# Kernel tuning notes

Hardware: AMD Instinct MI355X
Metric: run time of the kernel (lower is better)

The kernel has to match this reference:

```python
import jax, jax.numpy as jnp
import numpy as np

OBS, SEQ = 8, 12          # observed steps, predicted steps (seq_len init arg)
G, P = 96, 16             # scenes x pedestrians per scene (uniform groups)
B = G * P                 # 1536
H, E, BOT, MID = 128, 64, 1024, 512


def setup_inputs() -> dict:
    key = jax.random.key(0)
    ks = jax.random.split(key, 26)
    rn = lambda k, sh, s=0.05: jax.random.normal(k, sh, jnp.float32) * s
    starts = jnp.arange(G, dtype=jnp.int64) * P
    return {
        "obs_traj": rn(ks[0], (OBS, B, 2), 1.0),
        "obs_traj_rel": rn(ks[1], (OBS, B, 2), 1.0),
        "typeID_seq": rn(ks[2], (OBS, B, 1), 1.0),
        "h0": rn(ks[3], (1, B, H), 0.1),
        "c0": rn(ks[4], (1, B, H), 0.1),
        "seq_start_end": jnp.stack([starts, starts + P], axis=1),
        # decoder spatial embedding Linear(2, E)
        "W_emb": rn(ks[5], (E, 2)), "b_emb": rn(ks[6], (E,)),
        # LSTM(E, H) weights, gate order i,f,g,o (PyTorch convention)
        "W_ih": rn(ks[7], (4 * H, E)), "b_ih": rn(ks[8], (4 * H,)),
        "W_hh": rn(ks[9], (4 * H, H)), "b_hh": rn(ks[10], (4 * H,)),
        # hidden2pos Linear(H, 2)
        "W_pos": rn(ks[11], (2, H)), "b_pos": rn(ks[12], (2,)),
        # PoolHiddenNet: spatial_embedding Linear(2, E), mlp_pre_pool [E+H, 512, BOT]
        "Wp_emb": rn(ks[13], (E, 2)), "bp_emb": rn(ks[14], (E,)),
        "Wp1": rn(ks[15], (MID, E + H)), "bp1": rn(ks[16], (MID,)),
        "Wp2": rn(ks[17], (BOT, MID)), "bp2": rn(ks[18], (BOT,)),
        # Decoder mlp [H+BOT, mlp_dim, H]
        "Wm1": rn(ks[19], (1024, H + BOT)), "bm1": rn(ks[20], (1024,)),
        "Wm2": rn(ks[21], (H, 1024)), "bm2": rn(ks[22], (H,)),
    }


def _forward(obs_traj, obs_traj_rel, h0, c0,
             W_emb, b_emb, W_ih, b_ih, W_hh, b_hh, W_pos, b_pos,
             Wp_emb, bp_emb, Wp1, bp1, Wp2, bp2, Wm1, bm1, Wm2, bm2):
    batch = obs_traj.shape[1]

    def pool(h, pos):
        # uniform groups: h_states.view(-1,H)[start:end] == reshape to (G,P,H)
        hh = h.reshape(G, P, H)
        pp = pos.reshape(G, P, 2)
        # torch semantics: row (i,j) holds pos[j]-pos[i] and hidden[j]
        rel = pp[:, None, :, :] - pp[:, :, None, :]          # (G,Pi,Pj,2)
        emb = rel @ Wp_emb.T + bp_emb                        # (G,Pi,Pj,E)
        hb = jnp.broadcast_to(hh[:, None, :, :], (G, P, P, H))
        x = jnp.concatenate([emb, hb], axis=-1)              # (G,Pi,Pj,E+H)
        x = jax.nn.relu(x @ Wp1.T + bp1)
        x = jax.nn.relu(x @ Wp2.T + bp2)                     # (G,Pi,Pj,BOT)
        return x.max(axis=2).reshape(batch, BOT)             # max over neighbors j

    def step(carry, _):
        h, c, last_pos, dec_in = carry
        gates = dec_in @ W_ih.T + b_ih + h @ W_hh.T + b_hh
        i, f, g, o = jnp.split(gates, 4, axis=-1)
        c = jax.nn.sigmoid(f) * c + jax.nn.sigmoid(i) * jnp.tanh(g)
        h = jax.nn.sigmoid(o) * jnp.tanh(c)
        rel_pos = h @ W_pos.T + b_pos                        # (B,2)
        curr_pos = rel_pos + last_pos
        pool_h = pool(h, curr_pos)
        ctx = jnp.concatenate([h, pool_h], axis=-1)          # (B,H+BOT)
        h = jax.nn.relu(jax.nn.relu(ctx @ Wm1.T + bm1) @ Wm2.T + bm2)
        dec_in = rel_pos @ W_emb.T + b_emb
        return (h, c, curr_pos, dec_in), rel_pos

    dec_in0 = obs_traj_rel[-1] @ W_emb.T + b_emb
    carry0 = (h0[0], c0[0], obs_traj[-1], dec_in0)
    (h, c, _, _), rels = jax.lax.scan(step, carry0, None, length=SEQ)
    return rels, h[None]                                     # (SEQ,B,2), (1,B,H)


def reference(obs_traj, obs_traj_rel, typeID_seq, h0, c0, seq_start_end,
              W_emb, b_emb, W_ih, b_ih, W_hh, b_hh, W_pos, b_pos,
              Wp_emb, bp_emb, Wp1, bp1, Wp2, bp2, Wm1, bm1, Wm2, bm2):
    # typeID_seq / seq_start_end unused math-wise (typeID module off; groups uniform)
    return _forward(obs_traj, obs_traj_rel, h0, c0,
                    W_emb, b_emb, W_ih, b_ih, W_hh, b_hh, W_pos, b_pos,
                    Wp_emb, bp_emb, Wp1, bp1, Wp2, bp2, Wm1, bm1, Wm2, bm2)
```

## Files before the change

### kernel.cpp

```cpp
#include <hip/hip_runtime.h>
#include <hip/hip_bf16.h>
#include <math.h>

#define OBS 8
#define SEQL 12
#define G 96
#define PP 16
#define B 1536
#define HD 128
#define ED 64
#define BOT 1024
#define MIDD 512
#define CTXD (HD + BOT)
#define MLPH 1024

typedef __attribute__((ext_vector_type(8))) short bf16x8;
typedef __attribute__((ext_vector_type(4))) float f32x4;

__device__ inline short f2bf(float x) {
    union { float f; unsigned u; } v; v.f = x;
    unsigned r = v.u + 0x7fffu + ((v.u >> 16) & 1u);
    return (short)(r >> 16);
}

__device__ inline unsigned pk2bf(float a, float b) {
    union { __hip_bfloat162 h; unsigned u; } c;
    c.h = __float22bfloat162_rn(float2{a, b});
    return c.u;
}

__global__ void swizzleB_kernel(const float* __restrict__ src, unsigned short* __restrict__ dst,
                                int NT, int K, int total) {
    int u = blockIdx.x * 256 + threadIdx.x;
    if (u >= total) return;
    int l = u & 63; int v = u >> 6; int nt = v % NT; int kt = v / NT;
    int n = nt * 16 + (l & 15);
    int k = kt * 32 + ((l >> 4) << 3);
    const float* s = src + n * K + k;
    float4 s0 = *(const float4*)s;
    float4 s1 = *(const float4*)(s + 4);
    bf16x8 o;
    o[0] = f2bf(s0.x); o[1] = f2bf(s0.y); o[2] = f2bf(s0.z); o[3] = f2bf(s0.w);
    o[4] = f2bf(s1.x); o[5] = f2bf(s1.y); o[6] = f2bf(s1.z); o[7] = f2bf(s1.w);
    *(bf16x8*)(dst + u * 8) = o;
}

__global__ void swizzle_cat_kernel(const float* __restrict__ W_ih, const float* __restrict__ W_hh,
                                   unsigned short* __restrict__ dst) {
    int u = blockIdx.x * 256 + threadIdx.x;
    if (u >= 6 * 32 * 64) return;
    int l = u & 63; int v = u >> 6; int nt = v & 31; int kt = v >> 5;
    int n = nt * 16 + (l & 15);
    int k0 = kt * 32 + ((l >> 4) << 3);
    bf16x8 o;
#pragma unroll
    for (int e = 0; e < 8; ++e) {
        int k = k0 + e;
        float val = (k < ED) ? W_ih[n * ED + k] : W_hh[n * HD + (k - ED)];
        o[e] = f2bf(val);
    }
    *(bf16x8*)(dst + u * 8) = o;
}

__global__ void swizzle_p1_kernel(const float* __restrict__ Wp1,
                                  const float* __restrict__ CV,
                                  unsigned short* __restrict__ dst) {
    int u = blockIdx.x * 256 + threadIdx.x;
    if (u >= 5 * 32 * 64) return;
    int l = u & 63; int v = u >> 6; int nt = v & 31; int kt = v >> 5;
    int n = nt * 16 + (l & 15);
    int k0 = kt * 32 + ((l >> 4) << 3);
    bf16x8 o;
#pragma unroll
    for (int e = 0; e < 8; ++e) {
        int k = k0 + e;
        float val;
        if (k < HD)           val = Wp1[n * (ED + HD) + ED + k];
        else if (k == HD + 2) val = CV[n];
        else                  val = 0.f;
        o[e] = f2bf(val);
    }
    *(bf16x8*)(dst + u * 8) = o;
}

__global__ void mcvec_kernel(const float* __restrict__ Wp1, const float* __restrict__ Wp_emb,
                             const float* __restrict__ bp_emb, const float* __restrict__ bp1,
                             float* __restrict__ M0, float* __restrict__ M1, float* __restrict__ CV) {
    int r = blockIdx.x * blockDim.x + threadIdx.x;
    if (r >= MIDD) return;
    float m0 = 0.f, m1 = 0.f, cv = 0.f;
    for (int e = 0; e < ED; ++e) {
        float w = Wp1[r * (ED + HD) + e];
        m0 += w * Wp_emb[e * 2 + 0];
        m1 += w * Wp_emb[e * 2 + 1];
        cv += w * bp_emb[e];
    }
    M0[r] = m0; M1[r] = m1; CV[r] = cv + bp1[r];
}

__global__ void m01f_kernel(const float* __restrict__ M0, const float* __restrict__ M1,
                            float* __restrict__ M0F, float* __restrict__ M1F) {
    int id = blockIdx.x * 256 + threadIdx.x;
    if (id >= 16 * 64 * 8) return;
    int e = id & 7;
    int lane = (id >> 3) & 63;
    int kt = id >> 9;
    int k = kt * 32 + ((lane >> 4) << 3) + e;
    M0F[id] = M0[k];
    M1F[id] = M1[k];
}

__global__ void init_kernel(const float* __restrict__ obs_traj, const float* __restrict__ obs_traj_rel,
                            const float* __restrict__ h0, const float* __restrict__ c0,
                            const float* __restrict__ W_emb, const float* __restrict__ b_emb,
                            float* __restrict__ Hb, float* __restrict__ Cb,
                            float* __restrict__ POSb, float* __restrict__ DIN) {
    int b = blockIdx.x;
    int t = threadIdx.x;
    Hb[b * HD + t] = h0[b * HD + t];
    Cb[b * HD + t] = c0[b * HD + t];
    if (t < 2) POSb[b * 2 + t] = obs_traj[((OBS - 1) * B + b) * 2 + t];
    if (t < ED) {
        float rx = obs_traj_rel[((OBS - 1) * B + b) * 2 + 0];
        float ry = obs_traj_rel[((OBS - 1) * B + b) * 2 + 1];
        DIN[b * ED + t] = W_emb[t * 2 + 0] * rx + W_emb[t * 2 + 1] * ry + b_emb[t];
    }
}

__global__ __launch_bounds__(512) void step_kernel(
    const unsigned short* __restrict__ WcatF, const float* __restrict__ b_ih,
    const float* __restrict__ b_hh,
    const float* __restrict__ W_pos, const float* __restrict__ b_pos,
    const float* __restrict__ W_emb, const float* __restrict__ b_emb,
    const unsigned short* __restrict__ Wp1F2,
    float* __restrict__ Hb, float* __restrict__ Cb, float* __restrict__ POSb,
    float* __restrict__ DIN, unsigned short* __restrict__ Hbf,
    float* __restrict__ AbF, float* __restrict__ rel_out) {

    __shared__ unsigned short gf[6 * 64 * 8];
    __shared__ unsigned short a2f[5 * 64 * 8];
    __shared__ float hsh[16 * HD];
    __shared__ float relsh[16][4];

    int gsc = blockIdx.x;
    int t = threadIdx.x;
    int lane = t & 63, w = t >> 6;
    int colid = lane & 15, quad = lane >> 4;

    if (t < 384) {
        int kt = t >> 6;
        int j = lane & 15;
        int b = gsc * PP + j;
        int k0 = kt * 32 + ((lane >> 4) << 3);
        float4 x0, x1;
        if (k0 < ED) {
            const float4* p = (const float4*)(DIN + b * ED + k0);
            x0 = p[0]; x1 = p[1];
        } else {
            const float4* p = (const float4*)(Hb + b * HD + (k0 - ED));
            x0 = p[0]; x1 = p[1];
        }
        union { bf16x8 v; unsigned u32[4]; } o;
        o.u32[0] = pk2bf(x0.x, x0.y);
        o.u32[1] = pk2bf(x0.z, x0.w);
        o.u32[2] = pk2bf(x1.x, x1.y);
        o.u32[3] = pk2bf(x1.z, x1.w);
        *(bf16x8*)(gf + t * 8) = o.v;
    }
    __syncthreads();

    f32x4 acc[4];
#pragma unroll
    for (int gi = 0; gi < 4; ++gi) acc[gi] = (f32x4)0.f;
#pragma unroll
    for (int kt = 0; kt < 6; ++kt) {
        bf16x8 af = *(const bf16x8*)(gf + (kt * 64 + lane) * 8);
#pragma unroll
        for (int gi = 0; gi < 4; ++gi) {
            bf16x8 bfr = *(const bf16x8*)(WcatF + ((kt * 32 + gi * 8 + w) * 64 + lane) * 8);
            acc[gi] = __builtin_amdgcn_mfma_f32_16x16x32_bf16(af, bfr, acc[gi], 0, 0, 0);
        }
    }
    int hcol = w * 16 + colid;
    float bias[4];
#pragma unroll
    for (int gi = 0; gi < 4; ++gi) {
        int n = (gi * 8 + w) * 16 + colid;
        bias[gi] = b_ih[n] + b_hh[n];
    }
#pragma unroll
    for (int r = 0; r < 4; ++r) {
        int row = quad * 4 + r;
        int b = gsc * PP + row;
        float gI = acc[0][r] + bias[0];
        float gF = acc[1][r] + bias[1];
        float gG = acc[2][r] + bias[2];
        float gO = acc[3][r] + bias[3];
        float c = Cb[b * HD + hcol];
        float cn = (1.f / (1.f + expf(-gF))) * c + (1.f / (1.f + expf(-gI))) * tanhf(gG);
        float hn = (1.f / (1.f + expf(-gO))) * tanhf(cn);
        Cb[b * HD + hcol] = cn;
        Hbf[b * HD + hcol] = (unsigned short)f2bf(hn);
        hsh[row * HD + hcol] = hn;
    }
    __syncthreads();

    {
        int row = t >> 5, kk = t & 31;
        float r0 = 0.f, r1 = 0.f;
#pragma unroll
        for (int q = 0; q < 4; ++q) {
            int k = kk + q * 32;
            float hv = hsh[row * HD + k];
            r0 = fmaf(hv, W_pos[k], r0);
            r1 = fmaf(hv, W_pos[HD + k], r1);
        }
#pragma unroll
        for (int m = 16; m >= 1; m >>= 1) {
            r0 += __shfl_xor(r0, m, 64);
            r1 += __shfl_xor(r1, m, 64);
        }
        if (kk == 0) {
            int b = gsc * PP + row;
            r0 += b_pos[0]; r1 += b_pos[1];
            float px = POSb[b * 2 + 0] + r0;
            float py = POSb[b * 2 + 1] + r1;
            POSb[b * 2 + 0] = px; POSb[b * 2 + 1] = py;
            rel_out[b * 2 + 0] = r0; rel_out[b * 2 + 1] = r1;
            relsh[row][0] = r0; relsh[row][1] = r1; relsh[row][2] = px; relsh[row][3] = py;
        }
    }
    __syncthreads();

#pragma unroll
    for (int rep = 0; rep < 2; ++rep) {
        int idx = rep * 512 + t;
        int row = idx >> 6, e = idx & 63;
        int b = gsc * PP + row;
        DIN[b * ED + e] = W_emb[e * 2 + 0] * relsh[row][0] +
                          W_emb[e * 2 + 1] * relsh[row][1] + b_emb[e];
    }
    if (t < 320) {
        int kt = t >> 6;
        int j = lane & 15;
        int k0 = kt * 32 + ((lane >> 4) << 3);
        float e8[8];
#pragma unroll
        for (int e = 0; e < 8; ++e) {
            int k = k0 + e;
            float v;
            if (k < HD)            v = hsh[j * HD + k];
            else if (k == HD + 2)  v = 1.f;
            else                   v = 0.f;
            e8[e] = v;
        }
        union { bf16x8 v; unsigned u32[4]; } o;
        o.u32[0] = pk2bf(e8[0], e8[1]);
        o.u32[1] = pk2bf(e8[2], e8[3]);
        o.u32[2] = pk2bf(e8[4], e8[5]);
        o.u32[3] = pk2bf(e8[6], e8[7]);
        *(bf16x8*)(a2f + t * 8) = o.v;
    }
    __syncthreads();

    f32x4 acc2[4];
#pragma unroll
    for (int q = 0; q < 4; ++q) acc2[q] = (f32x4)0.f;
#pragma unroll
    for (int kt = 0; kt < 5; ++kt) {
        bf16x8 af = *(const bf16x8*)(a2f + (kt * 64 + lane) * 8);
#pragma unroll
        for (int q = 0; q < 4; ++q) {
            bf16x8 bfr = *(const bf16x8*)(Wp1F2 + ((kt * 32 + w * 4 + q) * 64 + lane) * 8);
            acc2[q] = __builtin_amdgcn_mfma_f32_16x16x32_bf16(af, bfr, acc2[q], 0, 0, 0);
        }
    }
#pragma unroll
    for (int q = 0; q < 4; ++q)
#pragma unroll
        for (int r = 0; r < 4; ++r) {
            int j = quad * 4 + r;
            int k = (w * 4 + q) * 16 + colid;
            int kt2 = k >> 5, lk = (k >> 3) & 3, e = k & 7;
            AbF[((gsc * 16 + kt2) * 64 + lk * 16 + j) * 8 + e] = acc2[q][r];
        }
}

__global__ __launch_bounds__(256, 4) void pool_gemm13_kernel(
    const float* __restrict__ AbF, const float* __restrict__ POSb,
    const float* __restrict__ M0F, const float* __restrict__ M1F,
    const unsigned short* __restrict__ Wp2F, const float* __restrict__ bp2,
    unsigned short* __restrict__ POOLbf) {

    __shared__ __align__(16) unsigned short Bst[2][8 * 64 * 8];
    __shared__ __align__(16) float UMst[2][6][64 * 4];

    int bi = blockIdx.x;
    int g = bi % 96;
    int rest = bi / 96;
    int io = rest >> 3;
    int colq = rest & 7;
    int t = threadIdx.x, lane = t & 63, w = t >> 6;
    int i0 = io * 8 + w * 2;
    int j = lane & 15;
    int ntb = colq * 8;

    float pjx = POSb[(g * PP + j) * 2 + 0];
    float pjy = POSb[(g * PP + j) * 2 + 1];
    float dx[2], dy[2];
#pragma unroll
    for (int p = 0; p < 2; ++p) {
        int gi = g * PP + i0 + p;
        dx[p] = pjx - POSb[gi * 2 + 0];
        dy[p] = pjy - POSb[gi * 2 + 1];
    }

    const float* ag = AbF + (size_t)g * (16 * 64 * 8);

    auto stage = [&](int kt, int buf) {
#pragma unroll
        for (int r = 0; r < 2; ++r) {
            int u = r * 256 + t;
            int nt = u >> 6, l = u & 63;
            *(bf16x8*)&Bst[buf][u * 8] =
                *(const bf16x8*)(Wp2F + ((kt * 64 + ntb + nt) * 64 + l) * 8);
        }
        {
            int pt = t >> 6;
            int l = t & 63;
            const float* src = (pt < 2) ? (ag + kt * 512 + l * 8 + pt * 4)
                                        : (M0F + kt * 512 + l * 8 + (pt - 2) * 4);
            *(float4*)&UMst[buf][pt][l * 4] = *(const float4*)src;
            if (t < 128) {
                int pt2 = 4 + (t >> 6);
                *(float4*)&UMst[buf][pt2][l * 4] =
                    *(const float4*)(M1F + kt * 512 + l * 8 + (t >> 6) * 4);
            }
        }
    };

    f32x4 acc[2][8];
#pragma unroll
    for (int p = 0; p < 2; ++p)
#pragma unroll
        for (int n = 0; n < 8; ++n) acc[p][n] = (f32x4)0.f;

    stage(0, 0);
    __syncthreads();

    for (int kt = 0; kt < 16; ++kt) {
        int buf = kt & 1;
        if (kt < 15) stage(kt + 1, buf ^ 1);

        float4 u0  = *(const float4*)&UMst[buf][0][lane * 4];
        float4 u1  = *(const float4*)&UMst[buf][1][lane * 4];
        float4 m00 = *(const float4*)&UMst[buf][2][lane * 4];
        float4 m01 = *(const float4*)&UMst[buf][3][lane * 4];
        float4 m10 = *(const float4*)&UMst[buf][4][lane * 4];
        float4 m11 = *(const float4*)&UMst[buf][5][lane * 4];

        bf16x8 af[2];
#pragma unroll
        for (int p = 0; p < 2; ++p) {
            float dxp = dx[p], dyp = dy[p];
            float r0 = fmaxf(fmaf(m10.x, dyp, fmaf(m00.x, dxp, u0.x)), 0.f);
            float r1 = fmaxf(fmaf(m10.y, dyp, fmaf(m00.y, dxp, u0.y)), 0.f);
            float r2 = fmaxf(fmaf(m10.z, dyp, fmaf(m00.z, dxp, u0.z)), 0.f);
            float r3 = fmaxf(fmaf(m10.w, dyp, fmaf(m00.w, dxp, u0.w)), 0.f);
            float r4 = fmaxf(fmaf(m11.x, dyp, fmaf(m01.x, dxp, u1.x)), 0.f);
            float r5 = fmaxf(fmaf(m11.y, dyp, fmaf(m01.y, dxp, u1.y)), 0.f);
            float r6 = fmaxf(fmaf(m11.z, dyp, fmaf(m01.z, dxp, u1.z)), 0.f);
            float r7 = fmaxf(fmaf(m11.w, dyp, fmaf(m01.w, dxp, u1.w)), 0.f);
            union { bf16x8 v; unsigned u32[4]; } o;
            o.u32[0] = pk2bf(r0, r1);
            o.u32[1] = pk2bf(r2, r3);
            o.u32[2] = pk2bf(r4, r5);
            o.u32[3] = pk2bf(r6, r7);
            af[p] = o.v;
        }
#pragma unroll
        for (int ng = 0; ng < 2; ++ng) {
            bf16x8 bfr[4];
#pragma unroll
            for (int n = 0; n < 4; ++n)
                bfr[n] = *(const bf16x8*)&Bst[buf][((ng * 4 + n) * 64 + lane) * 8];
#pragma unroll
            for (int n = 0; n < 4; ++n) {
                acc[0][ng * 4 + n] =
                    __builtin_amdgcn_mfma_f32_16x16x32_bf16(af[0], bfr[n], acc[0][ng * 4 + n], 0, 0, 0);
                acc[1][ng * 4 + n] =
                    __builtin_amdgcn_mfma_f32_16x16x32_bf16(af[1], bfr[n], acc[1][ng * 4 + n], 0, 0, 0);
            }
        }
        __syncthreads();
    }

    int quad = lane >> 4, colid = lane & 15;
#pragma unroll
    for (int p = 0; p < 2; ++p) {
        int i = g * PP + i0 + p;
#pragma unroll
        for (int n = 0; n < 8; ++n) {
            float m = fmaxf(fmaxf(acc[p][n][0], acc[p][n][1]),
                            fmaxf(acc[p][n][2], acc[p][n][3]));
            m = fmaxf(m, __shfl_xor(m, 16, 64));
            m = fmaxf(m, __shfl_xor(m, 32, 64));
            if (quad == 0) {
                int col = (ntb + n) * 16 + colid;
                float v = fmaxf(m + bp2[col], 0.f);
                POOLbf[i * BOT + col] = (unsigned short)f2bf(v);
            }
        }
    }
}

__global__ __launch_bounds__(256) void mlp1_mfma_kernel(
    const unsigned short* __restrict__ Hbf, const unsigned short* __restrict__ POOLbf,
    const unsigned short* __restrict__ Wm1F, const float* __restrict__ bm1,
    unsigned short* __restrict__ Y1Mbf) {

    __shared__ unsigned short a_f[16 * 64 * 8];
    int mg = blockIdx.x;
    int ng = blockIdx.y;
    int t = threadIdx.x, lane = t & 63, w = t >> 6;
    int rh = w >> 1, nh = w & 1;

    f32x4 acc[2][2];
#pragma unroll
    for (int a = 0; a < 2; ++a)
#pragma unroll
        for (int b = 0; b < 2; ++b) acc[a][b] = (f32x4)0.f;

    for (int c = 0; c < 9; ++c) {
        __syncthreads();
#pragma unroll
        for (int u0 = 0; u0 < 1024; u0 += 256) {
            int u = u0 + t;
            int rg = u >> 8, kt = (u >> 6) & 3, l = u & 63;
            int row = mg * 64 + rg * 16 + (l & 15);
            int kl = kt * 32 + ((l >> 4) << 3);
            const unsigned short* src = (c == 0) ? (Hbf + row * HD + kl)
                                                 : (POOLbf + row * BOT + (c - 1) * 128 + kl);
            *(bf16x8*)(a_f + u * 8) = *(const bf16x8*)src;
        }
        __syncthreads();
#pragma unroll
        for (int kt = 0; kt < 4; ++kt) {
            int ktg = c * 4 + kt;
            bf16x8 bfr[2];
#pragma unroll
            for (int j = 0; j < 2; ++j) {
                int ntg = ng * 4 + nh * 2 + j;
                bfr[j] = *(const bf16x8*)(Wm1F + ((ktg * 64 + ntg) * 64 + lane) * 8);
            }
#pragma unroll
            for (int ri = 0; ri < 2; ++ri) {
                int rg = rh * 2 + ri;
                bf16x8 af = *(const bf16x8*)(a_f + ((rg * 4 + kt) * 64 + lane) * 8);
#pragma unroll
                for (int j = 0; j < 2; ++j)
                    acc[ri][j] = __builtin_amdgcn_mfma_f32_16x16x32_bf16(af, bfr[j], acc[ri][j], 0, 0, 0);
            }
        }
    }
    int quad = lane >> 4, colid = lane & 15;
#pragma unroll
    for (int ri = 0; ri < 2; ++ri)
#pragma unroll
        for (int j = 0; j < 2; ++j) {
            int col = ng * 64 + (nh * 2 + j) * 16 + colid;
            float bb = bm1[col];
#pragma unroll
            for (int r = 0; r < 4; ++r) {
                int row = mg * 64 + (rh * 2 + ri) * 16 + quad * 4 + r;
                float v = fmaxf(acc[ri][j][r] + bb, 0.f);
                Y1Mbf[row * MLPH + col] = (unsigned short)f2bf(v);
            }
        }
}

__global__ __launch_bounds__(256) void mlp2_mfma_kernel(
    const unsigned short* __restrict__ Y1Mbf, const unsigned short* __restrict__ Wm2F,
    const float* __restrict__ bm2, float* __restrict__ Hb, float* __restrict__ hout) {

    __shared__ unsigned short a_f[32 * 64 * 8];
    int rg = blockIdx.x;
    int t = threadIdx.x, lane = t & 63, w = t >> 6;

#pragma unroll
    for (int u0 = 0; u0 < 2048; u0 += 256) {
        int u = u0 + t;
        int kt = u >> 6, l = u & 63;
        int row = rg * 16 + (l & 15);
        int kl = kt * 32 + ((l >> 4) << 3);
        *(bf16x8*)(a_f + u * 8) = *(const bf16x8*)(Y1Mbf + row * MLPH + kl);
    }
    __syncthreads();

    f32x4 acc[2];
    acc[0] = (f32x4)0.f; acc[1] = (f32x4)0.f;
    for (int kt = 0; kt < 32; ++kt) {
        bf16x8 af = *(const bf16x8*)(a_f + (kt * 64 + lane) * 8);
#pragma unroll
        for (int j = 0; j < 2; ++j) {
            int ntg = w * 2 + j;
            bf16x8 bfr = *(const bf16x8*)(Wm2F + ((kt * 8 + ntg) * 64 + lane) * 8);
            acc[j] = __builtin_amdgcn_mfma_f32_16x16x32_bf16(af, bfr, acc[j], 0, 0, 0);
        }
    }
    int quad = lane >> 4, colid = lane & 15;
#pragma unroll
    for (int j = 0; j < 2; ++j) {
        int col = (w * 2 + j) * 16 + colid;
        float bb = bm2[col];
#pragma unroll
        for (int r = 0; r < 4; ++r) {
            int row = rg * 16 + quad * 4 + r;
            float v = fmaxf(acc[j][r] + bb, 0.f);
            Hb[row * HD + col] = v;
            if (hout) hout[row * HD + col] = v;
        }
    }
}

extern "C" void kernel_launch(void* const* d_in, const int* in_sizes, int n_in,
                              void* d_out, int out_size, void* d_ws, size_t ws_size,
                              hipStream_t stream) {
    const float* obs_traj     = (const float*)d_in[0];
    const float* obs_traj_rel = (const float*)d_in[1];
    const float* h0    = (const float*)d_in[3];
    const float* c0    = (const float*)d_in[4];
    const float* W_emb = (const float*)d_in[6];
    const float* b_emb = (const float*)d_in[7];
    const float* W_ih  = (const float*)d_in[8];
    const float* b_ih  = (const float*)d_in[9];
    const float* W_hh  = (const float*)d_in[10];
    const float* b_hh  = (const float*)d_in[11];
    const float* W_pos = (const float*)d_in[12];
    const float* b_pos = (const float*)d_in[13];
    const float* Wp_emb= (const float*)d_in[14];
    const float* bp_emb= (const float*)d_in[15];
    const float* Wp1   = (const float*)d_in[16];
    const float* bp1   = (const float*)d_in[17];
    const float* Wp2   = (const float*)d_in[18];
    const float* bp2   = (const float*)d_in[19];
    const float* Wm1   = (const float*)d_in[20];
    const float* bm1   = (const float*)d_in[21];
    const float* Wm2   = (const float*)d_in[22];
    const float* bm2   = (const float*)d_in[23];

    float* ws = (float*)d_ws;
    float* Hb    = ws; ws += B * HD;
    float* Cb    = ws; ws += B * HD;
    float* POSb  = ws; ws += B * 2;
    float* DIN   = ws; ws += B * ED;
    float* AbF   = ws; ws += B * MIDD;
    float* M0    = ws; ws += MIDD;
    float* M1    = ws; ws += MIDD;
    float* CV    = ws; ws += MIDD;
    float* M0F   = ws; ws += 16 * 64 * 8;
    float* M1F   = ws; ws += 16 * 64 * 8;
    unsigned short* us = (unsigned short*)ws;
    unsigned short* Hbf    = us; us += B * HD;
    unsigned short* POOLbf = us; us += B * BOT;
    unsigned short* Y1Mbf  = us; us += B * MLPH;
    unsigned short* WcatF  = us; us += 6 * 32 * 64 * 8;
    unsigned short* Wp1F2  = us; us += 5 * 32 * 64 * 8;
    unsigned short* Wp2F   = us; us += MIDD * BOT;
    unsigned short* Wm1F   = us; us += CTXD * MLPH;
    unsigned short* Wm2F   = us; us += MLPH * HD;

    float* out = (float*)d_out;
    float* rels_out = out;
    float* h_out    = out + SEQL * B * 2;

    {
        int tot = 16 * 64 * 64;
        swizzleB_kernel<<<(tot + 255) / 256, 256, 0, stream>>>(Wp2, Wp2F, 64, MIDD, tot);
        tot = 36 * 64 * 64;
        swizzleB_kernel<<<(tot + 255) / 256, 256, 0, stream>>>(Wm1, Wm1F, 64, CTXD, tot);
        tot = 32 * 8 * 64;
        swizzleB_kernel<<<(tot + 255) / 256, 256, 0, stream>>>(Wm2, Wm2F, 8, MLPH, tot);
        swizzle_cat_kernel<<<(6 * 32 * 64 + 255) / 256, 256, 0, stream>>>(W_ih, W_hh, WcatF);
    }
    mcvec_kernel<<<2, 256, 0, stream>>>(Wp1, Wp_emb, bp_emb, bp1, M0, M1, CV);
    swizzle_p1_kernel<<<(5 * 32 * 64 + 255) / 256, 256, 0, stream>>>(Wp1, CV, Wp1F2);
    m01f_kernel<<<32, 256, 0, stream>>>(M0, M1, M0F, M1F);
    init_kernel<<<B, 128, 0, stream>>>(obs_traj, obs_traj_rel, h0, c0, W_emb, b_emb,
                                       Hb, Cb, POSb, DIN);

    for (int s = 0; s < SEQL; ++s) {
        step_kernel<<<G, 512, 0, stream>>>(
            WcatF, b_ih, b_hh, W_pos, b_pos, W_emb, b_emb, Wp1F2,
            Hb, Cb, POSb, DIN, Hbf, AbF, rels_out + s * B * 2);
        pool_gemm13_kernel<<<G * 16, 256, 0, stream>>>(AbF, POSb, M0F, M1F, Wp2F, bp2, POOLbf);
        mlp1_mfma_kernel<<<dim3(24, 16), 256, 0, stream>>>(Hbf, POOLbf, Wm1F, bm1, Y1Mbf);
        mlp2_mfma_kernel<<<G, 256, 0, stream>>>(Y1Mbf, Wm2F, bm2, Hb,
                                                (s == SEQL - 1) ? h_out : (float*)nullptr);
    }
}
```

Measured before the change: 1.094 ms.

## Fuse MLP second layer into next step's LSTM kernel

Moves the Wm2 projection and ReLU that produce the new hidden state into the start of the following step kernel, so each block computes its 16 rows of hidden state into shared memory and uses them directly. The separate mlp2 launch now runs only once after the loop to write the final hidden output. This removes 11 kernel launches and the global round trip of the hidden state between steps. In exchange the step kernel takes about 32KB more shared memory, which may reduce occupancy, and a single block size is used for the fused GEMM.

```diff
diff --git a/kernel.cpp b/kernel.cpp
--- a/kernel.cpp
+++ b/kernel.cpp
@@ -127,18 +127,22 @@
     }
 }
 
-__global__ __launch_bounds__(512) void step_kernel(
+__global__ __launch_bounds__(512) void fused_step_kernel(
+    const unsigned short* __restrict__ Y1Mbf, const unsigned short* __restrict__ Wm2F,
+    const float* __restrict__ bm2, const float* __restrict__ Hb, int first,
     const unsigned short* __restrict__ WcatF, const float* __restrict__ b_ih,
     const float* __restrict__ b_hh,
     const float* __restrict__ W_pos, const float* __restrict__ b_pos,
     const float* __restrict__ W_emb, const float* __restrict__ b_emb,
     const unsigned short* __restrict__ Wp1F2,
-    float* __restrict__ Hb, float* __restrict__ Cb, float* __restrict__ POSb,
+    float* __restrict__ Cb, float* __restrict__ POSb,
     float* __restrict__ DIN, unsigned short* __restrict__ Hbf,
     float* __restrict__ AbF, float* __restrict__ rel_out) {
 
+    __shared__ unsigned short y2f[32 * 64 * 8];
     __shared__ unsigned short gf[6 * 64 * 8];
     __shared__ unsigned short a2f[5 * 64 * 8];
+    __shared__ float hprev[16 * HD];
     __shared__ float hsh[16 * HD];
     __shared__ float relsh[16][4];
 
@@ -147,17 +151,50 @@
     int lane = t & 63, w = t >> 6;
     int colid = lane & 15, quad = lane >> 4;
 
+    if (!first) {
+#pragma unroll
+        for (int rep = 0; rep < 4; ++rep) {
+            int u = rep * 512 + t;
+            int kt = u >> 6, l = u & 63;
+            int row = gsc * PP + (l & 15);
+            int kl = kt * 32 + ((l >> 4) << 3);
+            *(bf16x8*)(y2f + u * 8) = *(const bf16x8*)(Y1Mbf + row * MLPH + kl);
+        }
+        __syncthreads();
+        f32x4 acch = (f32x4)0.f;
+        for (int kt = 0; kt < 32; ++kt) {
+            bf16x8 af = *(const bf16x8*)(y2f + (kt * 64 + lane) * 8);
+            bf16x8 bfr = *(const bf16x8*)(Wm2F + ((kt * 8 + w) * 64 + lane) * 8);
+            acch = __builtin_amdgcn_mfma_f32_16x16x32_bf16(af, bfr, acch, 0, 0, 0);
+        }
+        int hcol = w * 16 + colid;
+        float bb = bm2[hcol];
+#pragma unroll
+        for (int r = 0; r < 4; ++r) {
+            int row = quad * 4 + r;
+            hprev[row * HD + hcol] = fmaxf(acch[r] + bb, 0.f);
+        }
+    } else {
+#pragma unroll
+        for (int rep = 0; rep < 4; ++rep) {
+            int idx = rep * 512 + t;
+            int row = idx >> 7, col = idx & 127;
+            hprev[row * HD + col] = Hb[(gsc * PP + row) * HD + col];
+        }
+    }
+    __syncthreads();
+
     if (t < 384) {
         int kt = t >> 6;
         int j = lane & 15;
-        int b = gsc * PP + j;
         int k0 = kt * 32 + ((lane >> 4) << 3);
         float4 x0, x1;
         if (k0 < ED) {
+            int b = gsc * PP + j;
             const float4* p = (const float4*)(DIN + b * ED + k0);
             x0 = p[0]; x1 = p[1];
         } else {
-            const float4* p = (const float4*)(Hb + b * HD + (k0 - ED));
+            const float4* p = (const float4*)(hprev + j * HD + (k0 - ED));
             x0 = p[0]; x1 = p[1];
         }
         union { bf16x8 v; unsigned u32[4]; } o;
@@ -481,7 +518,7 @@
 
 __global__ __launch_bounds__(256) void mlp2_mfma_kernel(
     const unsigned short* __restrict__ Y1Mbf, const unsigned short* __restrict__ Wm2F,
-    const float* __restrict__ bm2, float* __restrict__ Hb, float* __restrict__ hout) {
+    const float* __restrict__ bm2, float* __restrict__ hout) {
 
     __shared__ unsigned short a_f[32 * 64 * 8];
     int rg = blockIdx.x;
@@ -516,9 +553,7 @@
 #pragma unroll
         for (int r = 0; r < 4; ++r) {
             int row = rg * 16 + quad * 4 + r;
-            float v = fmaxf(acc[j][r] + bb, 0.f);
-            Hb[row * HD + col] = v;
-            if (hout) hout[row * HD + col] = v;
+            hout[row * HD + col] = fmaxf(acc[j][r] + bb, 0.f);
         }
     }
 }
@@ -590,12 +625,12 @@
                                        Hb, Cb, POSb, DIN);
 
     for (int s = 0; s < SEQL; ++s) {
-        step_kernel<<<G, 512, 0, stream>>>(
+        fused_step_kernel<<<G, 512, 0, stream>>>(
+            Y1Mbf, Wm2F, bm2, Hb, (s == 0) ? 1 : 0,
             WcatF, b_ih, b_hh, W_pos, b_pos, W_emb, b_emb, Wp1F2,
-            Hb, Cb, POSb, DIN, Hbf, AbF, rels_out + s * B * 2);
+            Cb, POSb, DIN, Hbf, AbF, rels_out + s * B * 2);
         pool_gemm13_kernel<<<G * 16, 256, 0, stream>>>(AbF, POSb, M0F, M1F, Wp2F, bp2, POOLbf);
         mlp1_mfma_kernel<<<dim3(24, 16), 256, 0, stream>>>(Hbf, POOLbf, Wm1F, bm1, Y1Mbf);
-        mlp2_mfma_kernel<<<G, 256, 0, stream>>>(Y1Mbf, Wm2F, bm2, Hb,
-                                                (s == SEQL - 1) ? h_out : (float*)nullptr);
-    }
-}
+    }
+    mlp2_mfma_kernel<<<G, 256, 0, stream>>>(Y1Mbf, Wm2F, bm2, h_out);
+}
```

Result: faster. 1.060 ms (-3.1%).
